# Kernel tuning notes

Measured on AMD Instinct MI355X. Metric: run time of the kernel, lower is better.

The kernel has to match this reference:

```python
import jax, jax.numpy as jnp
import numpy as np

H = 512  # hidden_size
IN = 512  # input_size


def setup_inputs() -> dict:
    key = jax.random.key(0)
    ks = jax.random.split(key, 11)
    s = 1.0 / np.sqrt(H)
    T, B = 512, 256
    return {
        "x": jax.random.normal(ks[0], (T, B, IN), jnp.float32),
        "h0": jnp.zeros((B, H), jnp.float32),
        "g0": jnp.zeros((B, H), jnp.float32),
        # torch nn.Linear convention: y = x @ W.T + b, W ~ U(-1/sqrt(fan_in), ..)
        "Wx": jax.random.uniform(ks[1], (4 * H, IN), jnp.float32, -s, s),
        "bx": jax.random.uniform(ks[2], (4 * H,), jnp.float32, -s, s),
        "Wh": jax.random.uniform(ks[3], (3 * H, H), jnp.float32, -s, s),
        "bh": jax.random.uniform(ks[4], (3 * H,), jnp.float32, -s, s),
        "Wgh": jax.random.uniform(ks[5], (3 * H, H), jnp.float32, -s, s),
        "bgh": jax.random.uniform(ks[6], (3 * H,), jnp.float32, -s, s),
        "Whd": jax.random.uniform(ks[7], (3 * H, H), jnp.float32, -s, s),
        "bhd": jax.random.uniform(ks[8], (3 * H,), jnp.float32, -s, s),
        "Wg": jax.random.uniform(ks[9], (2 * H, H), jnp.float32, -s, s),
        "bg": jax.random.uniform(ks[10], (2 * H,), jnp.float32, -s, s),
    }


def _split(a, n):
    return jnp.split(a, n, axis=-1)


def reference(x, h0, g0, Wx, bx, Wh, bh, Wgh, bgh, Whd, bhd, Wg, bg):
    def step(carry, x_t):
        h, g = carry
        x_z, x_r, x_h, x_u = _split(x_t @ Wx.T + bx, 4)
        h_z, h_r, h_u = _split(h @ Wh.T + bh, 3)
        g_z, g_r, g_u = _split(g @ Wgh.T + bgh, 3)
        z = jax.nn.sigmoid(x_z + h_z + g_z)
        r = jax.nn.sigmoid(x_r + h_r + g_r)
        u = jax.nn.sigmoid(x_u + h_u + g_u)
        h_new = (1 - z) * h + z * jnp.tanh(x_h + r * h + u * g)
        h_d = h_new - h
        g_z2, g_r2 = _split(g @ Wg.T + bg, 2)
        hd_z, hd_r, hd_g = _split(h_d @ Whd.T + bhd, 3)
        z2 = jax.nn.sigmoid(hd_z + g_z2)
        r2 = jax.nn.sigmoid(hd_r + g_r2)
        g_new = (1 - z2) * g + z2 * jnp.tanh(hd_g + r2 * g)
        return (h_new, g_new), h_new

    (h, g), hs = jax.lax.scan(step, (h0, g0), x)
    return hs, h[None], g[None]
```

## Files before the change

### kernel.cpp

```cpp
#include <hip/hip_runtime.h>

#define Tn 512
#define Bn 256
#define Hn 512
#define INn 512
#define TPB 512

typedef __attribute__((ext_vector_type(8))) short bf16x8;
typedef __attribute__((ext_vector_type(4))) float f32x4;

__device__ __forceinline__ unsigned short f2bf(float f) {
  unsigned int u = __float_as_uint(f);
  unsigned int r = (u + 0x7fffu + ((u >> 16) & 1u)) >> 16;
  return (unsigned short)r;
}
__device__ __forceinline__ float bf2f(unsigned short u) {
  return __uint_as_float(((unsigned int)u) << 16);
}

__device__ __forceinline__ float sigm(float x) { return 1.0f / (1.0f + __expf(-x)); }
__device__ __forceinline__ float tanh_f(float x) { return 2.0f / (1.0f + __expf(-2.0f * x)) - 1.0f; }

__device__ __forceinline__ bf16x8 ld8(const unsigned short* p) {
  return *reinterpret_cast<const bf16x8*>(p);
}

__device__ __forceinline__ unsigned long long ald8(const unsigned short* p) {
  return __hip_atomic_load((const unsigned long long*)p, __ATOMIC_RELAXED,
                           __HIP_MEMORY_SCOPE_AGENT);
}
__device__ __forceinline__ void ast4(unsigned short* p, unsigned int v) {
  __hip_atomic_store((unsigned int*)p, v, __ATOMIC_RELAXED, __HIP_MEMORY_SCOPE_AGENT);
}
__device__ __forceinline__ unsigned int aldf(const unsigned int* p) {
  return __hip_atomic_load(p, __ATOMIC_RELAXED, __HIP_MEMORY_SCOPE_AGENT);
}
__device__ __forceinline__ void astf(unsigned int* p, unsigned int v) {
  __hip_atomic_store(p, v, __ATOMIC_RELAXED, __HIP_MEMORY_SCOPE_AGENT);
}

__device__ __forceinline__ f32x4 mfma16(bf16x8 a, bf16x8 b, f32x4 c) {
  return __builtin_amdgcn_mfma_f32_16x16x32_bf16(a, b, c, 0, 0, 0);
}

__global__ __launch_bounds__(256) void cvt_kernel(const float* __restrict__ in,
                                                  unsigned short* __restrict__ out, int n) {
  const int stride = gridDim.x * blockDim.x * 4;
  for (int i = (blockIdx.x * blockDim.x + threadIdx.x) * 4; i < n; i += stride) {
    float4 v = *reinterpret_cast<const float4*>(in + i);
    ushort4 o;
    o.x = f2bf(v.x); o.y = f2bf(v.y); o.z = f2bf(v.z); o.w = f2bf(v.w);
    *reinterpret_cast<ushort4*>(out + i) = o;
  }
}

__device__ __forceinline__ void xp_tile(const unsigned short* __restrict__ xb,
                                        const unsigned short* __restrict__ Wxb,
                                        unsigned short* dst, int tl, int b0,
                                        int j0, int gate, float biasv) {
  const int lane = threadIdx.x & 63;
  const int l15 = lane & 15;
  const int lk = (lane >> 4) * 8;
  const unsigned short* ap = xb + ((size_t)tl * Bn + b0 + l15) * INn + lk;
  const unsigned short* bp = Wxb + (size_t)(gate * 512 + j0 + l15) * INn + lk;
  f32x4 acc0 = {}, acc1 = {};
#pragma unroll
  for (int kt = 0; kt < 16; ++kt) {
    bf16x8 a0 = ld8(ap + kt * 32);
    bf16x8 a1 = ld8(ap + 16 * INn + kt * 32);
    bf16x8 bw = ld8(bp + kt * 32);
    acc0 = mfma16(a0, bw, acc0);
    acc1 = mfma16(a1, bw, acc1);
  }
#pragma unroll
  for (int r = 0; r < 4; ++r) {
    const int row = (lane >> 4) * 4 + r;
    dst[gate * 512 + row * 16 + l15] = f2bf(acc0[r] + biasv);
    dst[gate * 512 + (row + 16) * 16 + l15] = f2bf(acc1[r] + biasv);
  }
}

__device__ __forceinline__ void gather32(const unsigned short* src,
                                         unsigned short* dst, int b0) {
  const int lane = threadIdx.x & 63;
  const int w = threadIdx.x >> 6;
  const int c = (w << 3) + (lane & 7);
  const int r0 = (lane >> 3) << 2;
#pragma unroll
  for (int p = 0; p < 4; ++p) {
    const int rr = r0 + p;
    const unsigned short* s = src + (size_t)(b0 + rr) * Hn + c * 8;
    unsigned long long lo = ald8(s);
    unsigned long long hi = ald8(s + 4);
    char* d = (char*)dst + rr * 1024 + ((c * 16) ^ ((rr & 7) << 4));
    *(unsigned long long*)d = lo;
    *(unsigned long long*)(d + 8) = hi;
  }
}

__device__ __forceinline__ void poll_flags(const unsigned int* f, unsigned int ep,
                                           int jblk) {
  const int lane = threadIdx.x & 63;
  const int w = threadIdx.x >> 6;
  const int src = (w << 2) + ((lane & 7) >> 1);
  if (src == jblk) return;
  const unsigned int* p = f + src;
  while (aldf(p) < ep) __builtin_amdgcn_s_sleep(1);
}

__global__ __launch_bounds__(512, 1) void persist_kernel(
    const unsigned short* __restrict__ Whb,
    const unsigned short* __restrict__ Wghb,
    const unsigned short* __restrict__ Whdb,
    const unsigned short* __restrict__ Wgb,
    const unsigned short* __restrict__ xb,
    const unsigned short* __restrict__ Wxb,
    const float* __restrict__ bx,
    const float* __restrict__ bh,
    const float* __restrict__ bgh,
    const float* __restrict__ bhd,
    const float* __restrict__ bg,
    unsigned short* __restrict__ hb0,
    unsigned short* __restrict__ gb,
    unsigned short* __restrict__ hdb,
    float* __restrict__ g_master,
    const float* __restrict__ h0,
    const float* __restrict__ g0,
    float* __restrict__ hs,
    float* __restrict__ h_tail,
    float* __restrict__ g_tail,
    unsigned int* __restrict__ slab,
    int t0, int Tc) {
  __shared__ unsigned short Wh_l[48 * 512];
  __shared__ unsigned short As_h[32 * 512];
  __shared__ unsigned short As_B[32 * 512];
  __shared__ float pa[8][32][17];
  __shared__ unsigned short xp_ls[2][2048];

  const int tid = threadIdx.x;
  const int grp = blockIdx.x & 7;
  const int jblk = blockIdx.x >> 3;
  const int j0 = jblk * 16;
  const int b0 = grp * 32;
  const int wv = tid >> 6;
  const int lane = tid & 63;
  const int l15 = lane & 15;
  const int lk = (lane >> 4) * 8;
  unsigned int* FH = slab + grp * 64;
  unsigned int* FG = slab + grp * 64 + 32;

  for (int i = tid; i < 48 * 64; i += TPB) {
    const int rr = i >> 6, c = i & 63;
    const int grow = (rr >> 4) * 512 + j0 + (rr & 15);
    const int byte = rr * 1024 + ((c * 16) ^ ((rr & 7) << 4));
    *reinterpret_cast<uint4*>(reinterpret_cast<char*>(Wh_l) + byte) =
        *reinterpret_cast<const uint4*>(Whb + (size_t)grow * 512 + c * 8);
  }

  const int gx = wv & 3;
  const int jx = j0 + l15;
  float bxp = bx[gx * 512 + jx];
  if (gx == 0) bxp += bh[jx] + bgh[jx];
  else if (gx == 1) bxp += bh[512 + jx] + bgh[512 + jx];
  else if (gx == 3) bxp += bh[1024 + jx] + bgh[1024 + jx];

  if (wv < 4) xp_tile(xb, Wxb, &xp_ls[0][0], 0, b0, j0, gx, bxp);
  else if (Tc > 1) xp_tile(xb, Wxb, &xp_ls[1][0], 1, b0, j0, gx, bxp);

  const int bl_e = tid >> 4, jl_e = tid & 15;
  const int j_e = j0 + jl_e;
  const size_t o_e = (size_t)(b0 + bl_e) * Hn + j_e;
  float h_m = (t0 == 0) ? h0[o_e] : hs[(size_t)(t0 - 1) * (Bn * Hn) + o_e];
  float g_m = (t0 == 0) ? g0[o_e] : g_master[o_e];
  const float bz2 = bhd[j_e] + bg[j_e];
  const float br2 = bhd[512 + j_e] + bg[512 + j_e];
  const float bgc = bhd[1024 + j_e];
  const int xo = bl_e * 16 + jl_e;
  const int swzA = (l15 & 7) << 4;
  float z2p = 0.0f, r2p = 0.0f;

  gather32(hb0 + (size_t)(t0 & 1) * (Bn * Hn), As_h, b0);
  gather32(gb, As_B, b0);
  __syncthreads();
  {
    const unsigned short* As = (wv < 3) ? As_h : As_B;
    const unsigned short* bp =
        (wv < 3) ? nullptr
        : (wv < 6) ? Wghb + (size_t)((wv - 3) * 512 + j0 + l15) * Hn + lk
                   : Wgb + (size_t)((wv - 6) * 512 + j0 + l15) * Hn + lk;
    const int wrow = wv * 16 + l15;
    f32x4 acc0 = {}, acc1 = {};
#pragma unroll
    for (int kt = 0; kt < 16; ++kt) {
      const int k2 = (kt * 32 + lk) * 2;
      const int abyte = k2 ^ swzA;
      bf16x8 a0 = *reinterpret_cast<const bf16x8*>(
          reinterpret_cast<const char*>(As) + l15 * 1024 + abyte);
      bf16x8 a1 = *reinterpret_cast<const bf16x8*>(
          reinterpret_cast<const char*>(As) + (16 + l15) * 1024 + abyte);
      bf16x8 bw = (wv < 3)
          ? *reinterpret_cast<const bf16x8*>(
                reinterpret_cast<const char*>(Wh_l) + wrow * 1024 + (k2 ^ ((wrow & 7) << 4)))
          : ld8(bp + kt * 32);
      acc0 = mfma16(a0, bw, acc0);
      acc1 = mfma16(a1, bw, acc1);
    }
#pragma unroll
    for (int r = 0; r < 4; ++r) {
      pa[wv][(lane >> 4) * 4 + r][l15] = acc0[r];
      pa[wv][16 + (lane >> 4) * 4 + r][l15] = acc1[r];
    }
  }
  __syncthreads();
  {
    const float z = sigm(bf2f(xp_ls[0][xo]) + pa[0][bl_e][jl_e] + pa[3][bl_e][jl_e]);
    const float r = sigm(bf2f(xp_ls[0][512 + xo]) + pa[1][bl_e][jl_e] + pa[4][bl_e][jl_e]);
    const float u = sigm(bf2f(xp_ls[0][1536 + xo]) + pa[2][bl_e][jl_e] + pa[5][bl_e][jl_e]);
    const float cand = tanh_f(bf2f(xp_ls[0][1024 + xo]) + r * h_m + u * g_m);
    const float hn = (1.0f - z) * h_m + z * cand;
    const float hd = hn - h_m;
    hs[(size_t)t0 * (Bn * Hn) + o_e] = hn;
    const unsigned int hn_u = f2bf(hn), hd_u = f2bf(hd);
    const unsigned int hn_hi = (unsigned int)__shfl_down((int)hn_u, 1);
    const unsigned int hd_hi = (unsigned int)__shfl_down((int)hd_u, 1);
    if ((jl_e & 1) == 0) {
      ast4(hb0 + (size_t)((t0 + 1) & 1) * (Bn * Hn) + o_e, hn_u | (hn_hi << 16));
      ast4(hdb + o_e, hd_u | (hd_hi << 16));
    }
    z2p = pa[6][bl_e][jl_e];
    r2p = pa[7][bl_e][jl_e];
    h_m = hn;
  }
  __syncthreads();
  if (tid == 0) astf(FH + jblk, 1u);

  for (int tt = 0; tt < Tc; ++tt) {
    const int t = t0 + tt;

    poll_flags(FH, (unsigned int)(tt + 1), jblk);
    gather32(hb0 + (size_t)((t + 1) & 1) * (Bn * Hn), As_h, b0);
    gather32(hdb, As_B, b0);
    __syncthreads();
    if (wv < 3) {
      const int wrow = wv * 16 + l15;
      f32x4 acc0 = {}, acc1 = {};
#pragma unroll
      for (int kt = 0; kt < 16; ++kt) {
        const int k2 = (kt * 32 + lk) * 2;
        const int abyte = k2 ^ swzA;
        bf16x8 a0 = *reinterpret_cast<const bf16x8*>(
            reinterpret_cast<const char*>(As_h) + l15 * 1024 + abyte);
        bf16x8 a1 = *reinterpret_cast<const bf16x8*>(
            reinterpret_cast<const char*>(As_h) + (16 + l15) * 1024 + abyte);
        bf16x8 bw = *reinterpret_cast<const bf16x8*>(
            reinterpret_cast<const char*>(Wh_l) + wrow * 1024 + (k2 ^ ((wrow & 7) << 4)));
        acc0 = mfma16(a0, bw, acc0);
        acc1 = mfma16(a1, bw, acc1);
      }
#pragma unroll
      for (int r = 0; r < 4; ++r) {
        pa[wv][(lane >> 4) * 4 + r][l15] = acc0[r];
        pa[wv][16 + (lane >> 4) * 4 + r][l15] = acc1[r];
      }
    } else if (wv < 6) {
      const unsigned short* bp = Whdb + (size_t)((wv - 3) * 512 + j0 + l15) * Hn + lk;
      f32x4 acc0 = {}, acc1 = {};
#pragma unroll
      for (int kt = 0; kt < 16; ++kt) {
        const int k2 = (kt * 32 + lk) * 2;
        const int abyte = k2 ^ swzA;
        bf16x8 a0 = *reinterpret_cast<const bf16x8*>(
            reinterpret_cast<const char*>(As_B) + l15 * 1024 + abyte);
        bf16x8 a1 = *reinterpret_cast<const bf16x8*>(
            reinterpret_cast<const char*>(As_B) + (16 + l15) * 1024 + abyte);
        bf16x8 bw = ld8(bp + kt * 32);
        acc0 = mfma16(a0, bw, acc0);
        acc1 = mfma16(a1, bw, acc1);
      }
#pragma unroll
      for (int r = 0; r < 4; ++r) {
        pa[wv][(lane >> 4) * 4 + r][l15] = acc0[r];
        pa[wv][16 + (lane >> 4) * 4 + r][l15] = acc1[r];
      }
    }
    __syncthreads();
    {
      const float z2 = sigm(pa[3][bl_e][jl_e] + z2p + bz2);
      const float r2 = sigm(pa[4][bl_e][jl_e] + r2p + br2);
      const float gc = tanh_f(pa[5][bl_e][jl_e] + bgc + r2 * g_m);
      const float gn = (1.0f - z2) * g_m + z2 * gc;
      g_m = gn;
      if (t == Tn - 1) g_tail[o_e] = gn;
      const unsigned int gn_u = f2bf(gn);
      const unsigned int gn_hi = (unsigned int)__shfl_down((int)gn_u, 1);
      if ((jl_e & 1) == 0) ast4(gb + o_e, gn_u | (gn_hi << 16));
    }
    __syncthreads();
    if (tid == 0) astf(FG + jblk, (unsigned int)(tt + 1));

    if (tt + 1 >= Tc) break;

    if (wv < 4) {
      {
        const int src = (wv << 3) + (lane & 7);
        if (src != jblk) {
          const unsigned int* p = FG + src;
          while (aldf(p) < (unsigned int)(tt + 1)) __builtin_amdgcn_s_sleep(1);
        }
      }
      for (int p = 0; p < 8; ++p) {
        const int idx = tid + p * 256;
        const int rr = idx >> 6, c = idx & 63;
        const unsigned short* s = gb + (size_t)(b0 + rr) * Hn + c * 8;
        unsigned long long lo = ald8(s);
        unsigned long long hi = ald8(s + 4);
        char* d = (char*)As_B + rr * 1024 + ((c * 16) ^ ((rr & 7) << 4));
        *(unsigned long long*)d = lo;
        *(unsigned long long*)(d + 8) = hi;
      }
    } else if (tt + 2 < Tc) {
      xp_tile(xb, Wxb, &xp_ls[tt & 1][0], tt + 2, b0, j0, gx, bxp);
    }
    __syncthreads();
    if (wv < 3) {
      const unsigned short* bp = Wghb + (size_t)(wv * 512 + j0 + l15) * Hn + lk;
      f32x4 acc0 = {}, acc1 = {};
#pragma unroll
      for (int kt = 0; kt < 16; ++kt) {
        const int k2 = (kt * 32 + lk) * 2;
        const int abyte = k2 ^ swzA;
        bf16x8 a0 = *reinterpret_cast<const bf16x8*>(
            reinterpret_cast<const char*>(As_B) + l15 * 1024 + abyte);
        bf16x8 a1 = *reinterpret_cast<const bf16x8*>(
            reinterpret_cast<const char*>(As_B) + (16 + l15) * 1024 + abyte);
        bf16x8 bw = ld8(bp + kt * 32);
        acc0 = mfma16(a0, bw, acc0);
        acc1 = mfma16(a1, bw, acc1);
      }
#pragma unroll
      for (int r = 0; r < 4; ++r) {
        pa[3 + wv][(lane >> 4) * 4 + r][l15] = acc0[r];
        pa[3 + wv][16 + (lane >> 4) * 4 + r][l15] = acc1[r];
      }
    } else if (wv == 3) {
      const unsigned short* bp0 = Wgb + (size_t)(j0 + l15) * Hn + lk;
      const unsigned short* bp1 = Wgb + (size_t)(512 + j0 + l15) * Hn + lk;
      f32x4 a00 = {}, a01 = {}, a10 = {}, a11 = {};
#pragma unroll
      for (int kt = 0; kt < 16; ++kt) {
        const int k2 = (kt * 32 + lk) * 2;
        const int abyte = k2 ^ swzA;
        bf16x8 a0 = *reinterpret_cast<const bf16x8*>(
            reinterpret_cast<const char*>(As_B) + l15 * 1024 + abyte);
        bf16x8 a1 = *reinterpret_cast<const bf16x8*>(
            reinterpret_cast<const char*>(As_B) + (16 + l15) * 1024 + abyte);
        bf16x8 w0 = ld8(bp0 + kt * 32);
        bf16x8 w1 = ld8(bp1 + kt * 32);
        a00 = mfma16(a0, w0, a00);
        a10 = mfma16(a1, w0, a10);
        a01 = mfma16(a0, w1, a01);
        a11 = mfma16(a1, w1, a11);
      }
#pragma unroll
      for (int r = 0; r < 4; ++r) {
        pa[6][(lane >> 4) * 4 + r][l15] = a00[r];
        pa[6][16 + (lane >> 4) * 4 + r][l15] = a10[r];
        pa[7][(lane >> 4) * 4 + r][l15] = a01[r];
        pa[7][16 + (lane >> 4) * 4 + r][l15] = a11[r];
      }
    }
    __syncthreads();
    {
      const int xb_ = (tt + 1) & 1;
      const float z = sigm(bf2f(xp_ls[xb_][xo]) + pa[0][bl_e][jl_e] + pa[3][bl_e][jl_e]);
      const float r = sigm(bf2f(xp_ls[xb_][512 + xo]) + pa[1][bl_e][jl_e] + pa[4][bl_e][jl_e]);
      const float u = sigm(bf2f(xp_ls[xb_][1536 + xo]) + pa[2][bl_e][jl_e] + pa[5][bl_e][jl_e]);
      const float cand = tanh_f(bf2f(xp_ls[xb_][1024 + xo]) + r * h_m + u * g_m);
      const float hn = (1.0f - z) * h_m + z * cand;
      const float hd = hn - h_m;
      hs[(size_t)(t + 1) * (Bn * Hn) + o_e] = hn;
      if (t + 1 == Tn - 1) h_tail[o_e] = hn;
      const unsigned int hn_u = f2bf(hn), hd_u = f2bf(hd);
      const unsigned int hn_hi = (unsigned int)__shfl_down((int)hn_u, 1);
      const unsigned int hd_hi = (unsigned int)__shfl_down((int)hd_u, 1);
      if ((jl_e & 1) == 0) {
        ast4(hb0 + (size_t)(t & 1) * (Bn * Hn) + o_e, hn_u | (hn_hi << 16));
        ast4(hdb + o_e, hd_u | (hd_hi << 16));
      }
      z2p = pa[6][bl_e][jl_e];
      r2p = pa[7][bl_e][jl_e];
      h_m = hn;
    }
    __syncthreads();
    if (tid == 0) astf(FH + jblk, (unsigned int)(tt + 2));
  }
  g_master[o_e] = g_m;
}

extern "C" void kernel_launch(void* const* d_in, const int* in_sizes, int n_in,
                              void* d_out, int out_size, void* d_ws, size_t ws_size,
                              hipStream_t stream) {
  const float* x   = (const float*)d_in[0];
  const float* h0  = (const float*)d_in[1];
  const float* g0  = (const float*)d_in[2];
  const float* Wx  = (const float*)d_in[3];
  const float* bx  = (const float*)d_in[4];
  const float* Wh  = (const float*)d_in[5];
  const float* bh  = (const float*)d_in[6];
  const float* Wgh = (const float*)d_in[7];
  const float* bgh = (const float*)d_in[8];
  const float* Whd = (const float*)d_in[9];
  const float* bhd = (const float*)d_in[10];
  const float* Wg  = (const float*)d_in[11];
  const float* bg  = (const float*)d_in[12];

  char* ws = (char*)d_ws;
  unsigned short* Whb  = (unsigned short*)(ws + 0);
  unsigned short* Wghb = (unsigned short*)(ws + 1572864);
  unsigned short* Whdb = (unsigned short*)(ws + 3145728);
  unsigned short* Wgb  = (unsigned short*)(ws + 4718592);
  unsigned short* Wxb  = (unsigned short*)(ws + 5767168);
  unsigned short* hb0  = (unsigned short*)(ws + 7864320);
  unsigned short* gb_  = (unsigned short*)(ws + 8388608);
  unsigned short* hdb  = (unsigned short*)(ws + 8650752);
  float* g_master      = (float*)(ws + 8912896);
  unsigned int* flags  = (unsigned int*)(ws + 9437184);
  const size_t FIXED = 9453568ULL;

  int Tc = 512;
  while (Tc > 1 && FIXED + (size_t)Tc * 262144ULL > ws_size) Tc >>= 1;
  unsigned short* xb = (unsigned short*)(ws + FIXED);

  float* hs = (float*)d_out;
  float* h_tail = hs + (size_t)Tn * Bn * Hn;
  float* g_tail = h_tail + (size_t)Bn * Hn;

  cvt_kernel<<<dim3(512), 256, 0, stream>>>(Wh, Whb, 1536 * 512);
  cvt_kernel<<<dim3(512), 256, 0, stream>>>(Wgh, Wghb, 1536 * 512);
  cvt_kernel<<<dim3(512), 256, 0, stream>>>(Whd, Whdb, 1536 * 512);
  cvt_kernel<<<dim3(512), 256, 0, stream>>>(Wg, Wgb, 1024 * 512);
  cvt_kernel<<<dim3(512), 256, 0, stream>>>(Wx, Wxb, 2048 * 512);
  cvt_kernel<<<dim3(128), 256, 0, stream>>>(h0, hb0, Bn * Hn);
  cvt_kernel<<<dim3(128), 256, 0, stream>>>(g0, gb_, Bn * Hn);

  const int nChunks = Tn / Tc;
  for (int c = 0; c < nChunks; ++c) {
    const int t0 = c * Tc;
    hipMemsetAsync(flags, 0, 2048, stream);
    cvt_kernel<<<dim3(2048), 256, 0, stream>>>(x + (size_t)t0 * Bn * INn, xb,
                                               Tc * Bn * INn);
    persist_kernel<<<dim3(256), dim3(TPB), 0, stream>>>(
        Whb, Wghb, Whdb, Wgb, xb, Wxb, bx, bh, bgh, bhd, bg, hb0, gb_, hdb,
        g_master, h0, g0, hs, h_tail, g_tail, flags, t0, Tc);
  }
}
```

Measured before the change: 9.635 ms.

## Derive h_delta locally from double-buffered h tiles instead of a global hd buffer

Each step no longer writes or gathers the bf16 hidden-delta buffer through global memory. Instead, the previous and current gathered h tiles are kept double-buffered in shared memory and their difference is computed locally. Wh is now read from global/L2 instead of a preloaded LDS copy, which frees LDS for the second h buffer. The initial h0/g0 bf16 conversion is folded into the kernel prologue. This trades global stores and gathers for an extra LDS pass and barrier per step. It changes rounding, because the delta is now computed from bf16-rounded h values, and Wh loads now come from cache rather than LDS.

```diff
diff --git a/kernel.cpp b/kernel.cpp
--- a/kernel.cpp
+++ b/kernel.cpp
@@ -5,31 +5,28 @@
 #define Hn 512
 #define INn 512
 #define TPB 512
+#define BnHn (Bn * Hn)
 
 typedef __attribute__((ext_vector_type(8))) short bf16x8;
 typedef __attribute__((ext_vector_type(4))) float f32x4;
-
-__device__ __forceinline__ unsigned short f2bf(float f) {
+typedef unsigned long long ull;
+typedef unsigned short us;
+
+__device__ __forceinline__ us f2bf(float f) {
   unsigned int u = __float_as_uint(f);
-  unsigned int r = (u + 0x7fffu + ((u >> 16) & 1u)) >> 16;
-  return (unsigned short)r;
-}
-__device__ __forceinline__ float bf2f(unsigned short u) {
+  return (us)((u + 0x7fffu + ((u >> 16) & 1u)) >> 16);
+}
+__device__ __forceinline__ float bf2f(us u) {
   return __uint_as_float(((unsigned int)u) << 16);
 }
-
 __device__ __forceinline__ float sigm(float x) { return 1.0f / (1.0f + __expf(-x)); }
 __device__ __forceinline__ float tanh_f(float x) { return 2.0f / (1.0f + __expf(-2.0f * x)) - 1.0f; }
-
-__device__ __forceinline__ bf16x8 ld8(const unsigned short* p) {
-  return *reinterpret_cast<const bf16x8*>(p);
-}
-
-__device__ __forceinline__ unsigned long long ald8(const unsigned short* p) {
-  return __hip_atomic_load((const unsigned long long*)p, __ATOMIC_RELAXED,
-                           __HIP_MEMORY_SCOPE_AGENT);
-}
-__device__ __forceinline__ void ast4(unsigned short* p, unsigned int v) {
+__device__ __forceinline__ bf16x8 ld8(const us* p) { return *reinterpret_cast<const bf16x8*>(p); }
+
+__device__ __forceinline__ ull ald8(const us* p) {
+  return __hip_atomic_load((const ull*)p, __ATOMIC_RELAXED, __HIP_MEMORY_SCOPE_AGENT);
+}
+__device__ __forceinline__ void ast4(us* p, unsigned int v) {
   __hip_atomic_store((unsigned int*)p, v, __ATOMIC_RELAXED, __HIP_MEMORY_SCOPE_AGENT);
 }
 __device__ __forceinline__ unsigned int aldf(const unsigned int* p) {
@@ -38,13 +35,12 @@
 __device__ __forceinline__ void astf(unsigned int* p, unsigned int v) {
   __hip_atomic_store(p, v, __ATOMIC_RELAXED, __HIP_MEMORY_SCOPE_AGENT);
 }
-
 __device__ __forceinline__ f32x4 mfma16(bf16x8 a, bf16x8 b, f32x4 c) {
   return __builtin_amdgcn_mfma_f32_16x16x32_bf16(a, b, c, 0, 0, 0);
 }
 
 __global__ __launch_bounds__(256) void cvt_kernel(const float* __restrict__ in,
-                                                  unsigned short* __restrict__ out, int n) {
+                                                  us* __restrict__ out, int n) {
   const int stride = gridDim.x * blockDim.x * 4;
   for (int i = (blockIdx.x * blockDim.x + threadIdx.x) * 4; i < n; i += stride) {
     float4 v = *reinterpret_cast<const float4*>(in + i);
@@ -54,15 +50,15 @@
   }
 }
 
-__device__ __forceinline__ void xp_tile(const unsigned short* __restrict__ xb,
-                                        const unsigned short* __restrict__ Wxb,
-                                        unsigned short* dst, int tl, int b0,
+__device__ __forceinline__ void xp_tile(const us* __restrict__ xb,
+                                        const us* __restrict__ Wxb,
+                                        us* dst, int tl, int b0,
                                         int j0, int gate, float biasv) {
   const int lane = threadIdx.x & 63;
   const int l15 = lane & 15;
   const int lk = (lane >> 4) * 8;
-  const unsigned short* ap = xb + ((size_t)tl * Bn + b0 + l15) * INn + lk;
-  const unsigned short* bp = Wxb + (size_t)(gate * 512 + j0 + l15) * INn + lk;
+  const us* ap = xb + ((size_t)tl * Bn + b0 + l15) * INn + lk;
+  const us* bp = Wxb + (size_t)(gate * 512 + j0 + l15) * INn + lk;
   f32x4 acc0 = {}, acc1 = {};
 #pragma unroll
   for (int kt = 0; kt < 16; ++kt) {
@@ -80,8 +76,7 @@
   }
 }
 
-__device__ __forceinline__ void gather32(const unsigned short* src,
-                                         unsigned short* dst, int b0) {
+__device__ __forceinline__ void gather32(const us* src, us* dst, int b0) {
   const int lane = threadIdx.x & 63;
   const int w = threadIdx.x >> 6;
   const int c = (w << 3) + (lane & 7);
@@ -89,12 +84,12 @@
 #pragma unroll
   for (int p = 0; p < 4; ++p) {
     const int rr = r0 + p;
-    const unsigned short* s = src + (size_t)(b0 + rr) * Hn + c * 8;
-    unsigned long long lo = ald8(s);
-    unsigned long long hi = ald8(s + 4);
+    const us* s = src + (size_t)(b0 + rr) * Hn + c * 8;
+    ull lo = ald8(s);
+    ull hi = ald8(s + 4);
     char* d = (char*)dst + rr * 1024 + ((c * 16) ^ ((rr & 7) << 4));
-    *(unsigned long long*)d = lo;
-    *(unsigned long long*)(d + 8) = hi;
+    *(ull*)d = lo;
+    *(ull*)(d + 8) = hi;
   }
 }
 
@@ -109,20 +104,19 @@
 }
 
 __global__ __launch_bounds__(512, 1) void persist_kernel(
-    const unsigned short* __restrict__ Whb,
-    const unsigned short* __restrict__ Wghb,
-    const unsigned short* __restrict__ Whdb,
-    const unsigned short* __restrict__ Wgb,
-    const unsigned short* __restrict__ xb,
-    const unsigned short* __restrict__ Wxb,
+    const us* __restrict__ Whb,
+    const us* __restrict__ Wghb,
+    const us* __restrict__ Whdb,
+    const us* __restrict__ Wgb,
+    const us* __restrict__ xb,
+    const us* __restrict__ Wxb,
     const float* __restrict__ bx,
     const float* __restrict__ bh,
     const float* __restrict__ bgh,
     const float* __restrict__ bhd,
     const float* __restrict__ bg,
-    unsigned short* __restrict__ hb0,
-    unsigned short* __restrict__ gb,
-    unsigned short* __restrict__ hdb,
+    us* __restrict__ hb0,
+    us* __restrict__ gb,
     float* __restrict__ g_master,
     const float* __restrict__ h0,
     const float* __restrict__ g0,
@@ -131,11 +125,10 @@
     float* __restrict__ g_tail,
     unsigned int* __restrict__ slab,
     int t0, int Tc) {
-  __shared__ unsigned short Wh_l[48 * 512];
-  __shared__ unsigned short As_h[32 * 512];
-  __shared__ unsigned short As_B[32 * 512];
+  __shared__ us As_h[2][32 * 512];
+  __shared__ us As_B[32 * 512];
   __shared__ float pa[8][32][17];
-  __shared__ unsigned short xp_ls[2][2048];
+  __shared__ us xp_ls[2][2048];
 
   const int tid = threadIdx.x;
   const int grp = blockIdx.x & 7;
@@ -149,14 +142,6 @@
   unsigned int* FH = slab + grp * 64;
   unsigned int* FG = slab + grp * 64 + 32;
 
-  for (int i = tid; i < 48 * 64; i += TPB) {
-    const int rr = i >> 6, c = i & 63;
-    const int grow = (rr >> 4) * 512 + j0 + (rr & 15);
-    const int byte = rr * 1024 + ((c * 16) ^ ((rr & 7) << 4));
-    *reinterpret_cast<uint4*>(reinterpret_cast<char*>(Wh_l) + byte) =
-        *reinterpret_cast<const uint4*>(Whb + (size_t)grow * 512 + c * 8);
-  }
-
   const int gx = wv & 3;
   const int jx = j0 + l15;
   float bxp = bx[gx * 512 + jx];
@@ -170,7 +155,7 @@
   const int bl_e = tid >> 4, jl_e = tid & 15;
   const int j_e = j0 + jl_e;
   const size_t o_e = (size_t)(b0 + bl_e) * Hn + j_e;
-  float h_m = (t0 == 0) ? h0[o_e] : hs[(size_t)(t0 - 1) * (Bn * Hn) + o_e];
+  float h_m = (t0 == 0) ? h0[o_e] : hs[(size_t)(t0 - 1) * BnHn + o_e];
   float g_m = (t0 == 0) ? g0[o_e] : g_master[o_e];
   const float bz2 = bhd[j_e] + bg[j_e];
   const float br2 = bhd[512 + j_e] + bg[512 + j_e];
@@ -179,16 +164,30 @@
   const int swzA = (l15 & 7) << 4;
   float z2p = 0.0f, r2p = 0.0f;
 
-  gather32(hb0 + (size_t)(t0 & 1) * (Bn * Hn), As_h, b0);
-  gather32(gb, As_B, b0);
+  {
+    const float* hsrc = (t0 == 0) ? h0 : hs + (size_t)(t0 - 1) * BnHn;
+    const float* gsrc = (t0 == 0) ? g0 : g_master;
+#pragma unroll
+    for (int q = 0; q < 8; ++q) {
+      const int f = tid + q * 512;
+      const int rr = f >> 7, c4 = f & 127;
+      const int byte = rr * 1024 + ((c4 * 8) ^ ((rr & 7) << 4));
+      float4 hv = *reinterpret_cast<const float4*>(hsrc + (size_t)(b0 + rr) * Hn + c4 * 4);
+      float4 gv = *reinterpret_cast<const float4*>(gsrc + (size_t)(b0 + rr) * Hn + c4 * 4);
+      ull hu = (ull)f2bf(hv.x) | ((ull)f2bf(hv.y) << 16) | ((ull)f2bf(hv.z) << 32) |
+               ((ull)f2bf(hv.w) << 48);
+      ull gu = (ull)f2bf(gv.x) | ((ull)f2bf(gv.y) << 16) | ((ull)f2bf(gv.z) << 32) |
+               ((ull)f2bf(gv.w) << 48);
+      *reinterpret_cast<ull*>(reinterpret_cast<char*>(As_h[1]) + byte) = hu;
+      *reinterpret_cast<ull*>(reinterpret_cast<char*>(As_B) + byte) = gu;
+    }
+  }
   __syncthreads();
   {
-    const unsigned short* As = (wv < 3) ? As_h : As_B;
-    const unsigned short* bp =
-        (wv < 3) ? nullptr
-        : (wv < 6) ? Wghb + (size_t)((wv - 3) * 512 + j0 + l15) * Hn + lk
-                   : Wgb + (size_t)((wv - 6) * 512 + j0 + l15) * Hn + lk;
-    const int wrow = wv * 16 + l15;
+    const us* As = (wv < 3) ? As_h[1] : As_B;
+    const us* Wsel = (wv < 3) ? Whb : (wv < 6) ? Wghb : Wgb;
+    const int off = (wv < 3) ? wv * 512 : (wv < 6) ? (wv - 3) * 512 : (wv - 6) * 512;
+    const us* bp = Wsel + (size_t)(off + j0 + l15) * Hn + lk;
     f32x4 acc0 = {}, acc1 = {};
 #pragma unroll
     for (int kt = 0; kt < 16; ++kt) {
@@ -198,10 +197,7 @@
           reinterpret_cast<const char*>(As) + l15 * 1024 + abyte);
       bf16x8 a1 = *reinterpret_cast<const bf16x8*>(
           reinterpret_cast<const char*>(As) + (16 + l15) * 1024 + abyte);
-      bf16x8 bw = (wv < 3)
-          ? *reinterpret_cast<const bf16x8*>(
-                reinterpret_cast<const char*>(Wh_l) + wrow * 1024 + (k2 ^ ((wrow & 7) << 4)))
-          : ld8(bp + kt * 32);
+      bf16x8 bw = ld8(bp + kt * 32);
       acc0 = mfma16(a0, bw, acc0);
       acc1 = mfma16(a1, bw, acc1);
     }
@@ -218,15 +214,12 @@
     const float u = sigm(bf2f(xp_ls[0][1536 + xo]) + pa[2][bl_e][jl_e] + pa[5][bl_e][jl_e]);
     const float cand = tanh_f(bf2f(xp_ls[0][1024 + xo]) + r * h_m + u * g_m);
     const float hn = (1.0f - z) * h_m + z * cand;
-    const float hd = hn - h_m;
-    hs[(size_t)t0 * (Bn * Hn) + o_e] = hn;
-    const unsigned int hn_u = f2bf(hn), hd_u = f2bf(hd);
+    hs[(size_t)t0 * BnHn + o_e] = hn;
+    if (t0 == Tn - 1) h_tail[o_e] = hn;
+    const unsigned int hn_u = f2bf(hn);
     const unsigned int hn_hi = (unsigned int)__shfl_down((int)hn_u, 1);
-    const unsigned int hd_hi = (unsigned int)__shfl_down((int)hd_u, 1);
-    if ((jl_e & 1) == 0) {
-      ast4(hb0 + (size_t)((t0 + 1) & 1) * (Bn * Hn) + o_e, hn_u | (hn_hi << 16));
-      ast4(hdb + o_e, hd_u | (hd_hi << 16));
-    }
+    if ((jl_e & 1) == 0)
+      ast4(hb0 + (size_t)((t0 + 1) & 1) * BnHn + o_e, hn_u | (hn_hi << 16));
     z2p = pa[6][bl_e][jl_e];
     r2p = pa[7][bl_e][jl_e];
     h_m = hn;
@@ -236,24 +229,39 @@
 
   for (int tt = 0; tt < Tc; ++tt) {
     const int t = t0 + tt;
+    const int cur = tt & 1, prv = cur ^ 1;
 
     poll_flags(FH, (unsigned int)(tt + 1), jblk);
-    gather32(hb0 + (size_t)((t + 1) & 1) * (Bn * Hn), As_h, b0);
-    gather32(hdb, As_B, b0);
+    gather32(hb0 + (size_t)((t + 1) & 1) * BnHn, As_h[cur], b0);
+    __syncthreads();
+#pragma unroll
+    for (int q = 0; q < 8; ++q) {
+      const int f = tid + q * 512;
+      const int rr = f >> 7, c8 = f & 127;
+      const int byte = rr * 1024 + ((c8 * 8) ^ ((rr & 7) << 4));
+      const ull va = *reinterpret_cast<const ull*>(reinterpret_cast<const char*>(As_h[cur]) + byte);
+      const ull vb = *reinterpret_cast<const ull*>(reinterpret_cast<const char*>(As_h[prv]) + byte);
+      ull o = 0;
+#pragma unroll
+      for (int i = 0; i < 4; ++i) {
+        const float d = bf2f((us)(va >> (16 * i))) - bf2f((us)(vb >> (16 * i)));
+        o |= (ull)f2bf(d) << (16 * i);
+      }
+      *reinterpret_cast<ull*>(reinterpret_cast<char*>(As_B) + byte) = o;
+    }
     __syncthreads();
     if (wv < 3) {
-      const int wrow = wv * 16 + l15;
+      const us* bp = Whb + (size_t)(wv * 512 + j0 + l15) * Hn + lk;
       f32x4 acc0 = {}, acc1 = {};
 #pragma unroll
       for (int kt = 0; kt < 16; ++kt) {
         const int k2 = (kt * 32 + lk) * 2;
         const int abyte = k2 ^ swzA;
         bf16x8 a0 = *reinterpret_cast<const bf16x8*>(
-            reinterpret_cast<const char*>(As_h) + l15 * 1024 + abyte);
+            reinterpret_cast<const char*>(As_h[cur]) + l15 * 1024 + abyte);
         bf16x8 a1 = *reinterpret_cast<const bf16x8*>(
-            reinterpret_cast<const char*>(As_h) + (16 + l15) * 1024 + abyte);
-        bf16x8 bw = *reinterpret_cast<const bf16x8*>(
-            reinterpret_cast<const char*>(Wh_l) + wrow * 1024 + (k2 ^ ((wrow & 7) << 4)));
+            reinterpret_cast<const char*>(As_h[cur]) + (16 + l15) * 1024 + abyte);
+        bf16x8 bw = ld8(bp + kt * 32);
         acc0 = mfma16(a0, bw, acc0);
         acc1 = mfma16(a1, bw, acc1);
       }
@@ -263,7 +271,7 @@
         pa[wv][16 + (lane >> 4) * 4 + r][l15] = acc1[r];
       }
     } else if (wv < 6) {
-      const unsigned short* bp = Whdb + (size_t)((wv - 3) * 512 + j0 + l15) * Hn + lk;
+      const us* bp = Whdb + (size_t)((wv - 3) * 512 + j0 + l15) * Hn + lk;
       f32x4 acc0 = {}, acc1 = {};
 #pragma unroll
       for (int kt = 0; kt < 16; ++kt) {
@@ -311,19 +319,19 @@
       for (int p = 0; p < 8; ++p) {
         const int idx = tid + p * 256;
         const int rr = idx >> 6, c = idx & 63;
-        const unsigned short* s = gb + (size_t)(b0 + rr) * Hn + c * 8;
-        unsigned long long lo = ald8(s);
-        unsigned long long hi = ald8(s + 4);
+        const us* s = gb + (size_t)(b0 + rr) * Hn + c * 8;
+        ull lo = ald8(s);
+        ull hi = ald8(s + 4);
         char* d = (char*)As_B + rr * 1024 + ((c * 16) ^ ((rr & 7) << 4));
-        *(unsigned long long*)d = lo;
-        *(unsigned long long*)(d + 8) = hi;
+        *(ull*)d = lo;
+        *(ull*)(d + 8) = hi;
       }
     } else if (tt + 2 < Tc) {
       xp_tile(xb, Wxb, &xp_ls[tt & 1][0], tt + 2, b0, j0, gx, bxp);
     }
     __syncthreads();
     if (wv < 3) {
-      const unsigned short* bp = Wghb + (size_t)(wv * 512 + j0 + l15) * Hn + lk;
+      const us* bp = Wghb + (size_t)(wv * 512 + j0 + l15) * Hn + lk;
       f32x4 acc0 = {}, acc1 = {};
 #pragma unroll
       for (int kt = 0; kt < 16; ++kt) {
@@ -343,8 +351,8 @@
         pa[3 + wv][16 + (lane >> 4) * 4 + r][l15] = acc1[r];
       }
     } else if (wv == 3) {
-      const unsigned short* bp0 = Wgb + (size_t)(j0 + l15) * Hn + lk;
-      const unsigned short* bp1 = Wgb + (size_t)(512 + j0 + l15) * Hn + lk;
+      const us* bp0 = Wgb + (size_t)(j0 + l15) * Hn + lk;
+      const us* bp1 = Wgb + (size_t)(512 + j0 + l15) * Hn + lk;
       f32x4 a00 = {}, a01 = {}, a10 = {}, a11 = {};
 #pragma unroll
       for (int kt = 0; kt < 16; ++kt) {
@@ -377,16 +385,12 @@
       const float u = sigm(bf2f(xp_ls[xb_][1536 + xo]) + pa[2][bl_e][jl_e] + pa[5][bl_e][jl_e]);
       const float cand = tanh_f(bf2f(xp_ls[xb_][1024 + xo]) + r * h_m + u * g_m);
       const float hn = (1.0f - z) * h_m + z * cand;
-      const float hd = hn - h_m;
-      hs[(size_t)(t + 1) * (Bn * Hn) + o_e] = hn;
+      hs[(size_t)(t + 1) * BnHn + o_e] = hn;
       if (t + 1 == Tn - 1) h_tail[o_e] = hn;
-      const unsigned int hn_u = f2bf(hn), hd_u = f2bf(hd);
+      const unsigned int hn_u = f2bf(hn);
       const unsigned int hn_hi = (unsigned int)__shfl_down((int)hn_u, 1);
-      const unsigned int hd_hi = (unsigned int)__shfl_down((int)hd_u, 1);
-      if ((jl_e & 1) == 0) {
-        ast4(hb0 + (size_t)(t & 1) * (Bn * Hn) + o_e, hn_u | (hn_hi << 16));
-        ast4(hdb + o_e, hd_u | (hd_hi << 16));
-      }
+      if ((jl_e & 1) == 0)
+        ast4(hb0 + (size_t)(t & 1) * BnHn + o_e, hn_u | (hn_hi << 16));
       z2p = pa[6][bl_e][jl_e];
       r2p = pa[7][bl_e][jl_e];
       h_m = hn;
@@ -415,21 +419,20 @@
   const float* bg  = (const float*)d_in[12];
 
   char* ws = (char*)d_ws;
-  unsigned short* Whb  = (unsigned short*)(ws + 0);
-  unsigned short* Wghb = (unsigned short*)(ws + 1572864);
-  unsigned short* Whdb = (unsigned short*)(ws + 3145728);
-  unsigned short* Wgb  = (unsigned short*)(ws + 4718592);
-  unsigned short* Wxb  = (unsigned short*)(ws + 5767168);
-  unsigned short* hb0  = (unsigned short*)(ws + 7864320);
-  unsigned short* gb_  = (unsigned short*)(ws + 8388608);
-  unsigned short* hdb  = (unsigned short*)(ws + 8650752);
-  float* g_master      = (float*)(ws + 8912896);
-  unsigned int* flags  = (unsigned int*)(ws + 9437184);
-  const size_t FIXED = 9453568ULL;
+  us* Whb  = (us*)(ws + 0);
+  us* Wghb = (us*)(ws + 1572864);
+  us* Whdb = (us*)(ws + 3145728);
+  us* Wgb  = (us*)(ws + 4718592);
+  us* Wxb  = (us*)(ws + 5767168);
+  us* hb0  = (us*)(ws + 7864320);
+  us* gb_  = (us*)(ws + 8388608);
+  float* g_master     = (float*)(ws + 8650752);
+  unsigned int* flags = (unsigned int*)(ws + 9175040);
+  const size_t FIXED = 9177088ULL;
 
   int Tc = 512;
   while (Tc > 1 && FIXED + (size_t)Tc * 262144ULL > ws_size) Tc >>= 1;
-  unsigned short* xb = (unsigned short*)(ws + FIXED);
+  us* xb = (us*)(ws + FIXED);
 
   float* hs = (float*)d_out;
   float* h_tail = hs + (size_t)Tn * Bn * Hn;
@@ -440,8 +443,6 @@
   cvt_kernel<<<dim3(512), 256, 0, stream>>>(Whd, Whdb, 1536 * 512);
   cvt_kernel<<<dim3(512), 256, 0, stream>>>(Wg, Wgb, 1024 * 512);
   cvt_kernel<<<dim3(512), 256, 0, stream>>>(Wx, Wxb, 2048 * 512);
-  cvt_kernel<<<dim3(128), 256, 0, stream>>>(h0, hb0, Bn * Hn);
-  cvt_kernel<<<dim3(128), 256, 0, stream>>>(g0, gb_, Bn * Hn);
 
   const int nChunks = Tn / Tc;
   for (int c = 0; c < nChunks; ++c) {
@@ -450,7 +451,7 @@
     cvt_kernel<<<dim3(2048), 256, 0, stream>>>(x + (size_t)t0 * Bn * INn, xb,
                                                Tc * Bn * INn);
     persist_kernel<<<dim3(256), dim3(TPB), 0, stream>>>(
-        Whb, Wghb, Whdb, Wgb, xb, Wxb, bx, bh, bgh, bhd, bg, hb0, gb_, hdb,
+        Whb, Wghb, Whdb, Wgb, xb, Wxb, bx, bh, bgh, bhd, bg, hb0, gb_,
         g_master, h0, g0, hs, h_tail, g_tail, flags, t0, Tc);
   }
 }
```

After: 10.44 ms. 1.08x slower.
